# Performance work log

Hardware: AMD Instinct MI355X
Metric: run time of the kernel (lower is better)

The kernel has to match this reference:

```python
import jax, jax.numpy as jnp
import numpy as np

SOS = 0
MAX_LENGTH = 64

N_LATENTS = 256
N_CHARACTERS = 128
N_HIDDENS = 1024
BATCH = 4096


def setup_inputs() -> dict:
    key = jax.random.key(0)
    ks = jax.random.split(key, 16)
    H, L, C = N_HIDDENS, N_LATENTS, N_CHARACTERS
    s = 0.02
    return {
        "z": jax.random.normal(ks[0], (BATCH, L), dtype=jnp.float32),
        "embed_w": jax.random.normal(ks[1], (C, H), dtype=jnp.float32) * s,
        "z2h_w": jax.random.normal(ks[2], (H, L), dtype=jnp.float32) * s,
        "z2h_b": jnp.zeros((H,), dtype=jnp.float32),
        "w_ih0": jax.random.normal(ks[3], (3 * H, H + L), dtype=jnp.float32) * s,
        "w_hh0": jax.random.normal(ks[4], (3 * H, H), dtype=jnp.float32) * s,
        "b_ih0": jnp.zeros((3 * H,), dtype=jnp.float32),
        "b_hh0": jnp.zeros((3 * H,), dtype=jnp.float32),
        "w_ih1": jax.random.normal(ks[5], (3 * H, H), dtype=jnp.float32) * s,
        "w_hh1": jax.random.normal(ks[6], (3 * H, H), dtype=jnp.float32) * s,
        "b_ih1": jnp.zeros((3 * H,), dtype=jnp.float32),
        "b_hh1": jnp.zeros((3 * H,), dtype=jnp.float32),
        "h2o_w": jax.random.normal(ks[7], (C, H + L), dtype=jnp.float32) * s,
        "h2o_b": jnp.zeros((C,), dtype=jnp.float32),
    }


def _gru_cell(x, h, w_ih, w_hh, b_ih, b_hh):
    # PyTorch GRUCell math. x: [B, I], h: [B, H]
    gi = x @ w_ih.T + b_ih  # [B, 3H]
    gh = h @ w_hh.T + b_hh  # [B, 3H]
    i_r, i_z, i_n = jnp.split(gi, 3, axis=1)
    h_r, h_z, h_n = jnp.split(gh, 3, axis=1)
    r = jax.nn.sigmoid(i_r + h_r)
    zg = jax.nn.sigmoid(i_z + h_z)
    n = jnp.tanh(i_n + r * h_n)
    return (1.0 - zg) * n + zg * h


def reference(z, embed_w, z2h_w, z2h_b,
              w_ih0, w_hh0, b_ih0, b_hh0,
              w_ih1, w_hh1, b_ih1, b_hh1,
              h2o_w, h2o_b):
    batch = z.shape[0]
    h0 = z @ z2h_w.T + z2h_b  # [B, H], replicated across both GRU layers

    def step(carry, _):
        c_in, h1, h2 = carry
        e = embed_w[c_in]                      # [B, H] embedding lookup
        e = e * jax.nn.sigmoid(e)              # swish
        x = jnp.concatenate([e, z], axis=1)    # [B, H+L]
        h1 = _gru_cell(x, h1, w_ih0, w_hh0, b_ih0, b_hh0)
        h2 = _gru_cell(h1, h2, w_ih1, w_hh1, b_ih1, b_hh1)
        out = jnp.concatenate([h2, z], axis=1) @ h2o_w.T + h2o_b  # [B, C]
        # argmax(log_softmax(out)) == argmax(out)
        sample = jnp.argmax(out, axis=1).astype(jnp.int32)
        return (sample, h1, h2), out

    c0 = jnp.full((batch,), SOS, dtype=jnp.int32)
    _, outs = jax.lax.scan(step, (c0, h0, h0), None, length=MAX_LENGTH)
    return jnp.transpose(outs, (1, 0, 2))  # [B, T, C]
```

## Files before the change

### kernel.cpp

```cpp
#include <hip/hip_runtime.h>
#include <hip/hip_bf16.h>
#include <stdint.h>
#include <stddef.h>

#define B_   4096
#define H_   1024
#define L_   256
#define C_   128
#define T_   64
#define H3_  3072

typedef unsigned short u16;
typedef __attribute__((ext_vector_type(8))) short bf16x8;
typedef __attribute__((ext_vector_type(4))) float f32x4;

typedef const void __attribute__((address_space(1)))* as1_cvp;
typedef void __attribute__((address_space(3)))* as3_vp;

__device__ __forceinline__ void gl2lds16(const void* g, void* l) {
  __builtin_amdgcn_global_load_lds((as1_cvp)g, (as3_vp)l, 16, 0, 0);
}

__device__ __forceinline__ float bf2f(u16 u) {
  union { float f; unsigned int i; } x; x.i = ((unsigned int)u) << 16; return x.f;
}
__device__ __forceinline__ u16 f2bf(float f) {
  union { float f; unsigned int i; } x; x.f = f;
  unsigned int r = x.i + 0x7fffu + ((x.i >> 16) & 1u);
  return (u16)(r >> 16);
}
__device__ __forceinline__ float sigm(float x) { return 1.f / (1.f + __expf(-x)); }
__device__ __forceinline__ float tanh_fast(float x) {
  float e = __expf(2.f * x); return 1.f - 2.f / (e + 1.f);
}

template<int OUT_MODE>
__device__ __forceinline__ void gemm_tile_body(
    u16* As, u16* Ws,
    const u16* __restrict__ A, int lda,
    const u16* __restrict__ W, int ldw,
    const float* __restrict__ bias,
    void* __restrict__ C0p, void* __restrict__ C1p, int ldc, int K,
    int m0, int n0)
{
  const int tid  = threadIdx.x;
  const int wave = tid >> 6, lane = tid & 63;
  const int wm = (wave >> 1) * 64, wn = (wave & 1) * 64;
  const int lrow = lane & 15, lq = lane >> 4;
  const int arow = wave * 8 + (lane >> 3);
  const int acol = (lane & 7) * 8;

  f32x4 acc[4][4] = {};

  const u16* Ag = A + (size_t)m0 * lda;
  const u16* Wg = W + (size_t)n0 * ldw;

  for (int k0 = 0; k0 < K; k0 += 64) {
    __syncthreads();
    #pragma unroll
    for (int rd = 0; rd < 4; rd++) {
      gl2lds16(Ag + (size_t)(rd * 32 + arow) * lda + (k0 + acol), As + rd * 2048 + wave * 512);
      gl2lds16(Wg + (size_t)(rd * 32 + arow) * ldw + (k0 + acol), Ws + rd * 2048 + wave * 512);
    }
    __syncthreads();
    #pragma unroll
    for (int kk = 0; kk < 64; kk += 32) {
      bf16x8 af[4], bw[4];
      #pragma unroll
      for (int i = 0; i < 4; i++)
        af[i] = *(const bf16x8*)&As[(wm + i * 16 + lrow) * 64 + kk + lq * 8];
      #pragma unroll
      for (int j = 0; j < 4; j++)
        bw[j] = *(const bf16x8*)&Ws[(wn + j * 16 + lrow) * 64 + kk + lq * 8];
      #pragma unroll
      for (int i = 0; i < 4; i++)
        #pragma unroll
        for (int j = 0; j < 4; j++)
          acc[i][j] = __builtin_amdgcn_mfma_f32_16x16x32_bf16(af[i], bw[j], acc[i][j], 0, 0, 0);
    }
  }

  #pragma unroll
  for (int j = 0; j < 4; j++) {
    const int col = n0 + wn + j * 16 + lrow;
    const float bv = bias ? bias[col] : 0.f;
    #pragma unroll
    for (int i = 0; i < 4; i++) {
      #pragma unroll
      for (int r = 0; r < 4; r++) {
        const int row = m0 + wm + i * 16 + lq * 4 + r;
        float v = acc[i][j][r] + bv;
        if (OUT_MODE == 0) {
          ((float*)C0p)[(size_t)row * ldc + col] = v;
        } else if (OUT_MODE == 1) {
          ((u16*)C0p)[(size_t)row * ldc + col] = f2bf(v);
        } else {
          u16 hv = f2bf(v);
          ((u16*)C0p)[(size_t)row * ldc + col] = hv;
          ((u16*)C1p)[(size_t)row * ldc + col] = hv;
        }
      }
    }
  }
}

template<int OUT_MODE>
__global__ __launch_bounds__(256) void gemm_bt(
    const u16* __restrict__ A, int lda,
    const u16* __restrict__ W, int ldw,
    const float* __restrict__ bias,
    void* __restrict__ C0p, void* __restrict__ C1p, int ldc, int K)
{
  __shared__ __align__(16) u16 As[128 * 64];
  __shared__ __align__(16) u16 Ws[128 * 64];
  gemm_tile_body<OUT_MODE>(As, Ws, A, lda, W, ldw, bias, C0p, C1p, ldc, K,
                           blockIdx.y * 128, blockIdx.x * 128);
}

__device__ __forceinline__ void out_body(
    u16* As, u16* Ws, int ob,
    const u16* __restrict__ h2, const u16* __restrict__ Wo,
    const float* __restrict__ Oz, float* __restrict__ outp,
    int* __restrict__ cnew, int t)
{
  const int tid = threadIdx.x, wave = tid >> 6, lane = tid & 63;
  const int b0 = ob * 64;
  const int lrow = lane & 15, lq = lane >> 4;
  const int arow = wave * 8 + (lane >> 3);
  const int acol = (lane & 7) * 8;
  f32x4 acc[8] = {};

  for (int k0 = 0; k0 < H_; k0 += 64) {
    __syncthreads();
    #pragma unroll
    for (int rd = 0; rd < 2; rd++)
      gl2lds16(h2 + (size_t)(b0 + rd * 32 + arow) * H_ + k0 + acol, As + rd * 2048 + wave * 512);
    #pragma unroll
    for (int rd = 0; rd < 4; rd++)
      gl2lds16(Wo + (size_t)(rd * 32 + arow) * H_ + k0 + acol, Ws + rd * 2048 + wave * 512);
    __syncthreads();
    #pragma unroll
    for (int kk = 0; kk < 64; kk += 32) {
      bf16x8 af = *(const bf16x8*)&As[(wave * 16 + lrow) * 64 + kk + lq * 8];
      #pragma unroll
      for (int j = 0; j < 8; j++) {
        bf16x8 bw = *(const bf16x8*)&Ws[(j * 16 + lrow) * 64 + kk + lq * 8];
        acc[j] = __builtin_amdgcn_mfma_f32_16x16x32_bf16(af, bw, acc[j], 0, 0, 0);
      }
    }
  }

  #pragma unroll
  for (int r = 0; r < 4; r++) {
    const int row = b0 + wave * 16 + lq * 4 + r;
    float mv = -3.4e38f; int mi = 0;
    #pragma unroll
    for (int j = 0; j < 8; j++) {
      const int col = j * 16 + lrow;
      float v = acc[j][r] + Oz[(size_t)row * C_ + col];
      outp[(size_t)row * (T_ * C_) + t * C_ + col] = v;
      if (v > mv) { mv = v; mi = col; }
    }
    #pragma unroll
    for (int off = 1; off < 16; off <<= 1) {
      float ov = __shfl_xor(mv, off);
      int   oi = __shfl_xor(mi, off);
      if (ov > mv || (ov == mv && oi < mi)) { mv = ov; mi = oi; }
    }
    if (lrow == 0) cnew[row] = mi;
  }
}

__global__ __launch_bounds__(256) void out_k(
    const u16* __restrict__ h2cur, const u16* __restrict__ Wo,
    const float* __restrict__ Oz, float* __restrict__ outp,
    int* __restrict__ cbuf, int t)
{
  __shared__ __align__(16) u16 As[64 * 64];
  __shared__ __align__(16) u16 Ws[128 * 64];
  out_body(As, Ws, blockIdx.x, h2cur, Wo, Oz, outp, cbuf, t);
}

template<bool PH2>
__device__ __forceinline__ void l3_phase(
    u16* As, u16* Ws,
    const u16* __restrict__ Ag, const u16* __restrict__ Wg, int j0,
    f32x4 acc[3][2][4], f32x4 accN[2][4])
{
  const int tid = threadIdx.x, wave = tid >> 6, lane = tid & 63;
  const int wmh = wave >> 1, wj = wave & 1;
  const int lrow = lane & 15, lq = lane >> 4;
  const int arow = wave * 8 + (lane >> 3);
  const int acol = (lane & 7) * 8;

  for (int k0 = 0; k0 < H_; k0 += 64) {
    __syncthreads();
    #pragma unroll
    for (int rd = 0; rd < 4; rd++)
      gl2lds16(Ag + (size_t)(rd * 32 + arow) * H_ + (k0 + acol), As + rd * 2048 + wave * 512);
    #pragma unroll
    for (int rd = 0; rd < 6; rd++)
      gl2lds16(Wg + (size_t)((rd >> 1) * 1024 + j0 + (rd & 1) * 32 + arow) * H_ + (k0 + acol),
               Ws + rd * 2048 + wave * 512);
    __syncthreads();
    #pragma unroll
    for (int kk = 0; kk < 64; kk += 32) {
      bf16x8 af[4];
      #pragma unroll
      for (int i = 0; i < 4; i++)
        af[i] = *(const bf16x8*)&As[(wmh * 64 + i * 16 + lrow) * 64 + kk + lq * 8];
      #pragma unroll
      for (int g = 0; g < 3; g++) {
        #pragma unroll
        for (int u = 0; u < 2; u++) {
          bf16x8 bw = *(const bf16x8*)&Ws[(g * 64 + wj * 32 + u * 16 + lrow) * 64 + kk + lq * 8];
          #pragma unroll
          for (int i = 0; i < 4; i++) {
            if (PH2 && g == 2)
              accN[u][i] = __builtin_amdgcn_mfma_f32_16x16x32_bf16(af[i], bw, accN[u][i], 0, 0, 0);
            else
              acc[g][u][i] = __builtin_amdgcn_mfma_f32_16x16x32_bf16(af[i], bw, acc[g][u][i], 0, 0, 0);
          }
        }
      }
    }
  }
}

__global__ __launch_bounds__(256, 2) void gemm_g1(
    const u16* __restrict__ h1old, const u16* __restrict__ whh0,
    const float* __restrict__ b_hh0,
    const int* __restrict__ cbuf, const u16* __restrict__ Egi,
    const u16* __restrict__ Gz, u16* __restrict__ h1new)
{
  __shared__ __align__(16) u16 As[128 * 64];
  __shared__ __align__(16) u16 Ws[192 * 64];
  const int bid = blockIdx.x;
  const int xcd = bid & 7, k = bid >> 3;
  const int jt = xcd * 2 + (k & 1);
  const int m  = k >> 1;
  const int m0 = m * 128, j0 = jt * 64;

  f32x4 acc[3][2][4] = {};
  f32x4 accN[2][4] = {};

  l3_phase<false>(As, Ws, h1old + (size_t)m0 * H_, whh0, j0, acc, accN);

  const int tid = threadIdx.x, wave = tid >> 6, lane = tid & 63;
  const int wmh = wave >> 1, wj = wave & 1;
  const int lrow = lane & 15, lq = lane >> 4;

  #pragma unroll
  for (int u = 0; u < 2; u++) {
    const int j = j0 + wj * 32 + u * 16 + lrow;
    const float bR = b_hh0[j];
    const float bZ = b_hh0[H_ + j];
    const float bN = b_hh0[2 * H_ + j];
    #pragma unroll
    for (int i = 0; i < 4; i++) {
      #pragma unroll
      for (int rr = 0; rr < 4; rr++) {
        const int row = m0 + wmh * 64 + i * 16 + lq * 4 + rr;
        const size_t eb = (size_t)cbuf[row] * H3_ + j;
        const size_t gb = (size_t)row * H3_ + j;
        float r  = sigm(bf2f(Egi[eb])           + bf2f(Gz[gb])           + acc[0][u][i][rr] + bR);
        float zg = sigm(bf2f(Egi[eb + H_])      + bf2f(Gz[gb + H_])      + acc[1][u][i][rr] + bZ);
        float nn = tanh_fast(bf2f(Egi[eb + 2 * H_]) + bf2f(Gz[gb + 2 * H_])
                             + r * (acc[2][u][i][rr] + bN));
        float hold = bf2f(h1old[(size_t)row * H_ + j]);
        h1new[(size_t)row * H_ + j] = f2bf((1.f - zg) * nn + zg * hold);
      }
    }
  }
}

__global__ __launch_bounds__(256, 2) void gemm_l3(
    const u16* __restrict__ h1, const u16* __restrict__ h2old,
    const u16* __restrict__ wih1, const u16* __restrict__ whh1,
    const float* __restrict__ b_ih1, const float* __restrict__ b_hh1,
    u16* __restrict__ h2new)
{
  __shared__ __align__(16) u16 As[128 * 64];
  __shared__ __align__(16) u16 Ws[192 * 64];
  const int bid = blockIdx.x;
  const int xcd = bid & 7, k = bid >> 3;
  const int jt = xcd * 2 + (k & 1);
  const int m  = k >> 1;
  const int m0 = m * 128, j0 = jt * 64;

  f32x4 acc[3][2][4] = {};
  f32x4 accN[2][4] = {};

  l3_phase<false>(As, Ws, h1    + (size_t)m0 * H_, wih1, j0, acc, accN);
  l3_phase<true >(As, Ws, h2old + (size_t)m0 * H_, whh1, j0, acc, accN);

  const int tid = threadIdx.x, wave = tid >> 6, lane = tid & 63;
  const int wmh = wave >> 1, wj = wave & 1;
  const int lrow = lane & 15, lq = lane >> 4;

  #pragma unroll
  for (int u = 0; u < 2; u++) {
    const int j = j0 + wj * 32 + u * 16 + lrow;
    const float bR  = b_ih1[j] + b_hh1[j];
    const float bZ  = b_ih1[H_ + j] + b_hh1[H_ + j];
    const float bNi = b_ih1[2 * H_ + j];
    const float bNh = b_hh1[2 * H_ + j];
    #pragma unroll
    for (int i = 0; i < 4; i++) {
      #pragma unroll
      for (int rr = 0; rr < 4; rr++) {
        const int row = m0 + wmh * 64 + i * 16 + lq * 4 + rr;
        float r  = sigm(acc[0][u][i][rr] + bR);
        float zg = sigm(acc[1][u][i][rr] + bZ);
        float nn = tanh_fast(acc[2][u][i][rr] + bNi + r * (accN[u][i][rr] + bNh));
        float hold = bf2f(h2old[(size_t)row * H_ + j]);
        h2new[(size_t)row * H_ + j] = f2bf((1.f - zg) * nn + zg * hold);
      }
    }
  }
}

__global__ __launch_bounds__(256) void conv_bf16_k(const float* __restrict__ s, u16* __restrict__ d, int n) {
  int i = blockIdx.x * 256 + threadIdx.x;
  if (i < n) d[i] = f2bf(s[i]);
}
__global__ __launch_bounds__(256) void conv_split_k(const float* __restrict__ s, u16* __restrict__ dA,
                                                    u16* __restrict__ dZ, int rows) {
  int i = blockIdx.x * 256 + threadIdx.x;
  if (i >= rows * 1280) return;
  int rr = i / 1280, col = i - rr * 1280;
  float v = s[i];
  if (col < 1024) dA[(size_t)rr * 1024 + col] = f2bf(v);
  else            dZ[(size_t)rr * 256 + (col - 1024)] = f2bf(v);
}
__global__ __launch_bounds__(256) void conv_swish_k(const float* __restrict__ s, u16* __restrict__ d, int n) {
  int i = blockIdx.x * 256 + threadIdx.x;
  if (i < n) { float e = s[i]; d[i] = f2bf(e * sigm(e)); }
}

static inline char* wsal(char*& p, size_t bytes) {
  char* r = p; p += (bytes + 255) & ~(size_t)255; return r;
}

extern "C" void kernel_launch(void* const* d_in, const int* in_sizes, int n_in,
                              void* d_out, int out_size, void* d_ws, size_t ws_size,
                              hipStream_t stream) {
  const float* z       = (const float*)d_in[0];
  const float* embed_w = (const float*)d_in[1];
  const float* z2h_w   = (const float*)d_in[2];
  const float* z2h_b   = (const float*)d_in[3];
  const float* w_ih0   = (const float*)d_in[4];
  const float* w_hh0   = (const float*)d_in[5];
  const float* b_ih0   = (const float*)d_in[6];
  const float* b_hh0   = (const float*)d_in[7];
  const float* w_ih1   = (const float*)d_in[8];
  const float* w_hh1   = (const float*)d_in[9];
  const float* b_ih1   = (const float*)d_in[10];
  const float* b_hh1   = (const float*)d_in[11];
  const float* h2o_w   = (const float*)d_in[12];
  const float* h2o_b   = (const float*)d_in[13];
  float* outp = (float*)d_out;

  char* p = (char*)d_ws;
  u16* whh0  = (u16*)wsal(p, (size_t)H3_ * H_ * 2);
  u16* wih1  = (u16*)wsal(p, (size_t)H3_ * H_ * 2);
  u16* whh1  = (u16*)wsal(p, (size_t)H3_ * H_ * 2);
  u16* wih0a = (u16*)wsal(p, (size_t)H3_ * H_ * 2);
  u16* wih0z = (u16*)wsal(p, (size_t)H3_ * L_ * 2);
  u16* h2oa  = (u16*)wsal(p, (size_t)C_ * H_ * 2);
  u16* h2oz  = (u16*)wsal(p, (size_t)C_ * L_ * 2);
  u16* z2hb  = (u16*)wsal(p, (size_t)H_ * L_ * 2);
  u16* zb    = (u16*)wsal(p, (size_t)B_ * L_ * 2);
  u16* swe   = (u16*)wsal(p, (size_t)C_ * H_ * 2);
  u16* EgiB  = (u16*)wsal(p, (size_t)C_ * H3_ * 2);
  u16* Gz    = (u16*)wsal(p, (size_t)B_ * H3_ * 2);
  float* Oz  = (float*)wsal(p, (size_t)B_ * C_ * 4);
  u16* h1a   = (u16*)wsal(p, (size_t)B_ * H_ * 2);
  u16* h1b   = (u16*)wsal(p, (size_t)B_ * H_ * 2);
  u16* h2a   = (u16*)wsal(p, (size_t)B_ * H_ * 2);
  u16* h2b   = (u16*)wsal(p, (size_t)B_ * H_ * 2);
  int* cbuf  = (int*)wsal(p, (size_t)B_ * 4);

  conv_bf16_k<<<(B_*L_ + 255)/256, 256, 0, stream>>>(z, zb, B_*L_);
  conv_bf16_k<<<(H_*L_ + 255)/256, 256, 0, stream>>>(z2h_w, z2hb, H_*L_);
  conv_bf16_k<<<(H3_*H_ + 255)/256, 256, 0, stream>>>(w_hh0, whh0, H3_*H_);
  conv_bf16_k<<<(H3_*H_ + 255)/256, 256, 0, stream>>>(w_ih1, wih1, H3_*H_);
  conv_bf16_k<<<(H3_*H_ + 255)/256, 256, 0, stream>>>(w_hh1, whh1, H3_*H_);
  conv_split_k<<<(H3_*1280 + 255)/256, 256, 0, stream>>>(w_ih0, wih0a, wih0z, H3_);
  conv_split_k<<<(C_*1280 + 255)/256, 256, 0, stream>>>(h2o_w, h2oa, h2oz, C_);
  conv_swish_k<<<(C_*H_ + 255)/256, 256, 0, stream>>>(embed_w, swe, C_*H_);
  hipMemsetAsync(cbuf, 0, B_ * sizeof(int), stream);

  gemm_bt<2><<<dim3(H_/128, B_/128), 256, 0, stream>>>(zb, L_, z2hb, L_, z2h_b, h1a, h2a, H_, L_);
  gemm_bt<1><<<dim3(H3_/128, 1), 256, 0, stream>>>(swe, H_, wih0a, H_, b_ih0, EgiB, nullptr, H3_, H_);
  gemm_bt<1><<<dim3(H3_/128, B_/128), 256, 0, stream>>>(zb, L_, wih0z, L_, nullptr, Gz, nullptr, H3_, L_);
  gemm_bt<0><<<dim3(1, B_/128), 256, 0, stream>>>(zb, L_, h2oz, L_, h2o_b, Oz, nullptr, C_, L_);

  for (int t = 0; t < T_; t++) {
    const u16* h2cur = (t & 1) ? h2b : h2a;
    u16*       h2nxt = (t & 1) ? h2a : h2b;
    const u16* h1cur = (t & 1) ? h1b : h1a;
    u16*       h1nxt = (t & 1) ? h1a : h1b;
    if (t > 0)
      out_k<<<64, 256, 0, stream>>>(h2cur, h2oa, Oz, outp, cbuf, t - 1);
    gemm_g1<<<512, 256, 0, stream>>>(h1cur, whh0, b_hh0, cbuf, EgiB, Gz, h1nxt);
    gemm_l3<<<512, 256, 0, stream>>>(h1nxt, h2cur, wih1, whh1, b_ih1, b_hh1, h2nxt);
  }
  out_k<<<64, 256, 0, stream>>>(h2a, h2oa, Oz, outp, cbuf, T_ - 1);
}
```

Baseline: 8.450 ms.

## Double-buffer GRU GEMM k-loop with 256-row tiles and swizzled LDS

Replaces the single-buffered GRU gate GEMMs with 512-thread blocks that each cover 256 batch rows. The k-loop now uses two LDS buffers filled by async global-to-LDS loads issued two tiles ahead, with explicit vmcnt waits, barriers and MFMA priority boosts. Layer 1's input-hidden and hidden-hidden phases are merged into one continuous pipelined loop. An XOR swizzle on LDS columns is added to reduce bank conflicts. The 112KB of LDS per block limits a CU to one block, and the grid shrinks to 256 blocks, so latency hiding relies on the prefetch pipeline rather than on multiple resident blocks.

```diff
diff --git a/kernel.cpp b/kernel.cpp
--- a/kernel.cpp
+++ b/kernel.cpp
@@ -181,70 +181,109 @@
   out_body(As, Ws, blockIdx.x, h2cur, Wo, Oz, outp, cbuf, t);
 }
 
+
+__device__ __forceinline__ void stage256(const u16* Ag, const u16* Wg, int k0,
+                                         u16* bA, u16* bW) {
+  const int tid = threadIdx.x;
+  const int wave = tid >> 6, lane = tid & 63;
+  const int r64 = wave * 8 + (lane >> 3);
+  const int cSw = (((lane & 7) ^ ((lane >> 5) << 1)) << 3);
+  #pragma unroll
+  for (int rd = 0; rd < 4; rd++)
+    gl2lds16(Ag + (size_t)(rd * 64 + r64) * H_ + k0 + cSw, bA + rd * 4096 + wave * 512);
+  #pragma unroll
+  for (int rd = 0; rd < 3; rd++)
+    gl2lds16(Wg + (size_t)(rd * 1024 + r64) * H_ + k0 + cSw, bW + rd * 4096 + wave * 512);
+}
+
 template<bool PH2>
-__device__ __forceinline__ void l3_phase(
-    u16* As, u16* Ws,
-    const u16* __restrict__ Ag, const u16* __restrict__ Wg, int j0,
-    f32x4 acc[3][2][4], f32x4 accN[2][4])
-{
-  const int tid = threadIdx.x, wave = tid >> 6, lane = tid & 63;
+__device__ __forceinline__ void tile_mfma(const u16* bA, const u16* bW,
+                                          f32x4 acc[3][2][4], f32x4 accN[2][4]) {
+  const int tid = threadIdx.x;
+  const int wave = tid >> 6, lane = tid & 63;
   const int wmh = wave >> 1, wj = wave & 1;
   const int lrow = lane & 15, lq = lane >> 4;
-  const int arow = wave * 8 + (lane >> 3);
-  const int acol = (lane & 7) * 8;
-
-  for (int k0 = 0; k0 < H_; k0 += 64) {
-    __syncthreads();
-    #pragma unroll
-    for (int rd = 0; rd < 4; rd++)
-      gl2lds16(Ag + (size_t)(rd * 32 + arow) * H_ + (k0 + acol), As + rd * 2048 + wave * 512);
-    #pragma unroll
-    for (int rd = 0; rd < 6; rd++)
-      gl2lds16(Wg + (size_t)((rd >> 1) * 1024 + j0 + (rd & 1) * 32 + arow) * H_ + (k0 + acol),
-               Ws + rd * 2048 + wave * 512);
-    __syncthreads();
-    #pragma unroll
-    for (int kk = 0; kk < 64; kk += 32) {
-      bf16x8 af[4];
-      #pragma unroll
-      for (int i = 0; i < 4; i++)
-        af[i] = *(const bf16x8*)&As[(wmh * 64 + i * 16 + lrow) * 64 + kk + lq * 8];
-      #pragma unroll
-      for (int g = 0; g < 3; g++) {
+  const int rsw = ((lrow >> 2) & 1) << 4;
+  #pragma unroll
+  for (int kk = 0; kk < 64; kk += 32) {
+    const int csw = (kk + lq * 8) ^ rsw;
+    bf16x8 af[4];
+    #pragma unroll
+    for (int i = 0; i < 4; i++)
+      af[i] = *(const bf16x8*)&bA[(wmh * 64 + i * 16 + lrow) * 64 + csw];
+    #pragma unroll
+    for (int g = 0; g < 3; g++) {
+      #pragma unroll
+      for (int u = 0; u < 2; u++) {
+        bf16x8 bw = *(const bf16x8*)&bW[(g * 64 + wj * 32 + u * 16 + lrow) * 64 + csw];
         #pragma unroll
-        for (int u = 0; u < 2; u++) {
-          bf16x8 bw = *(const bf16x8*)&Ws[(g * 64 + wj * 32 + u * 16 + lrow) * 64 + kk + lq * 8];
-          #pragma unroll
-          for (int i = 0; i < 4; i++) {
-            if (PH2 && g == 2)
-              accN[u][i] = __builtin_amdgcn_mfma_f32_16x16x32_bf16(af[i], bw, accN[u][i], 0, 0, 0);
-            else
-              acc[g][u][i] = __builtin_amdgcn_mfma_f32_16x16x32_bf16(af[i], bw, acc[g][u][i], 0, 0, 0);
-          }
+        for (int i = 0; i < 4; i++) {
+          if (PH2 && g == 2)
+            accN[u][i] = __builtin_amdgcn_mfma_f32_16x16x32_bf16(af[i], bw, accN[u][i], 0, 0, 0);
+          else
+            acc[g][u][i] = __builtin_amdgcn_mfma_f32_16x16x32_bf16(af[i], bw, acc[g][u][i], 0, 0, 0);
         }
       }
     }
   }
 }
 
-__global__ __launch_bounds__(256, 2) void gemm_g1(
+template<int NT, int P1T, bool DUAL>
+__device__ __forceinline__ void kloop256(
+    u16* As, u16* Ws,
+    const u16* A1g, const u16* W1g,
+    const u16* A2g, const u16* W2g,
+    f32x4 acc[3][2][4], f32x4 accN[2][4])
+{
+  stage256(A1g, W1g, 0, As, Ws);
+  if (P1T > 1) stage256(A1g, W1g, 64, As + 16384, Ws + 12288);
+  else         stage256(A2g, W2g, 0,  As + 16384, Ws + 12288);
+
+  #pragma unroll 2
+  for (int v = 0; v < NT; v++) {
+    u16* bA = (v & 1) ? As + 16384 : As;
+    u16* bW = (v & 1) ? Ws + 12288 : Ws;
+    if (v + 1 < NT) asm volatile("s_waitcnt vmcnt(7)" ::: "memory");
+    else            asm volatile("s_waitcnt vmcnt(0)" ::: "memory");
+    __builtin_amdgcn_sched_barrier(0);
+    __builtin_amdgcn_s_barrier();
+    __builtin_amdgcn_sched_barrier(0);
+    __builtin_amdgcn_s_setprio(1);
+    if (!DUAL || v < P1T) tile_mfma<false>(bA, bW, acc, accN);
+    else                  tile_mfma<true >(bA, bW, acc, accN);
+    __builtin_amdgcn_s_setprio(0);
+    __builtin_amdgcn_sched_barrier(0);
+    __builtin_amdgcn_s_barrier();
+    __builtin_amdgcn_sched_barrier(0);
+    const int w = v + 2;
+    if (w < NT) {
+      const u16* Av = (w < P1T) ? A1g : A2g;
+      const u16* Wv = (w < P1T) ? W1g : W2g;
+      const int k0 = ((w < P1T) ? w : w - P1T) * 64;
+      stage256(Av, Wv, k0, bA, bW);
+    }
+  }
+}
+
+__global__ __launch_bounds__(512, 2) void gru0_256(
     const u16* __restrict__ h1old, const u16* __restrict__ whh0,
-    const float* __restrict__ b_hh0,
-    const int* __restrict__ cbuf, const u16* __restrict__ Egi,
-    const u16* __restrict__ Gz, u16* __restrict__ h1new)
-{
-  __shared__ __align__(16) u16 As[128 * 64];
-  __shared__ __align__(16) u16 Ws[192 * 64];
+    const float* __restrict__ b_hh0, const int* __restrict__ cbuf,
+    const u16* __restrict__ Egi, const u16* __restrict__ Gz,
+    u16* __restrict__ h1new)
+{
+  __shared__ __align__(16) u16 As[2 * 16384];
+  __shared__ __align__(16) u16 Ws[2 * 12288];
   const int bid = blockIdx.x;
   const int xcd = bid & 7, k = bid >> 3;
   const int jt = xcd * 2 + (k & 1);
   const int m  = k >> 1;
-  const int m0 = m * 128, j0 = jt * 64;
+  const int m0 = m * 256, j0 = jt * 64;
 
   f32x4 acc[3][2][4] = {};
   f32x4 accN[2][4] = {};
-
-  l3_phase<false>(As, Ws, h1old + (size_t)m0 * H_, whh0, j0, acc, accN);
+  kloop256<16, 16, false>(As, Ws,
+                          h1old + (size_t)m0 * H_, whh0 + (size_t)j0 * H_,
+                          h1old, whh0, acc, accN);
 
   const int tid = threadIdx.x, wave = tid >> 6, lane = tid & 63;
   const int wmh = wave >> 1, wj = wave & 1;
@@ -274,25 +313,26 @@
   }
 }
 
-__global__ __launch_bounds__(256, 2) void gemm_l3(
+__global__ __launch_bounds__(512, 2) void gru1_256(
     const u16* __restrict__ h1, const u16* __restrict__ h2old,
     const u16* __restrict__ wih1, const u16* __restrict__ whh1,
     const float* __restrict__ b_ih1, const float* __restrict__ b_hh1,
     u16* __restrict__ h2new)
 {
-  __shared__ __align__(16) u16 As[128 * 64];
-  __shared__ __align__(16) u16 Ws[192 * 64];
+  __shared__ __align__(16) u16 As[2 * 16384];
+  __shared__ __align__(16) u16 Ws[2 * 12288];
   const int bid = blockIdx.x;
   const int xcd = bid & 7, k = bid >> 3;
   const int jt = xcd * 2 + (k & 1);
   const int m  = k >> 1;
-  const int m0 = m * 128, j0 = jt * 64;
+  const int m0 = m * 256, j0 = jt * 64;
 
   f32x4 acc[3][2][4] = {};
   f32x4 accN[2][4] = {};
-
-  l3_phase<false>(As, Ws, h1    + (size_t)m0 * H_, wih1, j0, acc, accN);
-  l3_phase<true >(As, Ws, h2old + (size_t)m0 * H_, whh1, j0, acc, accN);
+  kloop256<32, 16, true>(As, Ws,
+                         h1    + (size_t)m0 * H_, wih1 + (size_t)j0 * H_,
+                         h2old + (size_t)m0 * H_, whh1 + (size_t)j0 * H_,
+                         acc, accN);
 
   const int tid = threadIdx.x, wave = tid >> 6, lane = tid & 63;
   const int wmh = wave >> 1, wj = wave & 1;
@@ -403,8 +443,8 @@
     u16*       h1nxt = (t & 1) ? h1a : h1b;
     if (t > 0)
       out_k<<<64, 256, 0, stream>>>(h2cur, h2oa, Oz, outp, cbuf, t - 1);
-    gemm_g1<<<512, 256, 0, stream>>>(h1cur, whh0, b_hh0, cbuf, EgiB, Gz, h1nxt);
-    gemm_l3<<<512, 256, 0, stream>>>(h1nxt, h2cur, wih1, whh1, b_ih1, b_hh1, h2nxt);
+    gru0_256<<<256, 512, 0, stream>>>(h1cur, whh0, b_hh0, cbuf, EgiB, Gz, h1nxt);
+    gru1_256<<<256, 512, 0, stream>>>(h1nxt, h2cur, wih1, whh1, b_ih1, b_hh1, h2nxt);
   }
   out_k<<<64, 256, 0, stream>>>(h2a, h2oa, Oz, outp, cbuf, T_ - 1);
 }
```

Measured after the change: 14.03 ms. +66.0%, slower.
